# Kernel optimization log

Measured on AMD Instinct MI355X. Metric: run time of the kernel, lower is better.

The kernel has to match this reference:

```python
import jax, jax.numpy as jnp
import numpy as np
import math

N_HEADS = 12
D_MODEL = 768
D_HEAD = 64
IGNORE = -100000.0
INIT_STD = 0.02


def setup_inputs() -> dict:
    key = jax.random.key(0)
    ks = jax.random.split(key, 8)
    b, s = 4, 1024
    return {
        "normalized_resid_pre": jax.random.normal(ks[0], (b, 1, s, D_MODEL), jnp.float32),
        "alt_normalized_resid_pre": jax.random.normal(ks[1], (b, s, D_MODEL), jnp.float32),
        "W_Q": jax.random.normal(ks[2], (N_HEADS, D_MODEL, D_HEAD), jnp.float32) * INIT_STD,
        "b_Q": jnp.zeros((N_HEADS, D_HEAD), jnp.float32),
        "W_K": jax.random.normal(ks[3], (N_HEADS, D_MODEL, D_HEAD), jnp.float32) * INIT_STD,
        "b_K": jnp.zeros((N_HEADS, D_HEAD), jnp.float32),
        "W_V": jax.random.normal(ks[4], (N_HEADS, D_MODEL, D_HEAD), jnp.float32) * INIT_STD,
        "b_V": jnp.zeros((N_HEADS, D_HEAD), jnp.float32),
        "W_O": jax.random.normal(ks[5], (N_HEADS, D_HEAD, D_MODEL), jnp.float32) * INIT_STD,
        "b_O": jnp.zeros((D_MODEL,), jnp.float32),
    }


def _apply_attention(x, W_Q, b_Q, W_K, b_K, W_V, b_V, W_O):
    # x: [batch, n_prev(=2), seq, d_model]
    q = jnp.einsum('bpsd,ndh->bpsnh', x, W_Q) + b_Q
    k = jnp.einsum('bpsd,ndh->bpsnh', x, W_K) + b_K
    v = jnp.einsum('bpsd,ndh->bpsnh', x, W_V) + b_V
    scores = jnp.einsum('bpqnh,bpknh->bpnqk', q, k) / math.sqrt(D_HEAD)
    s = scores.shape[-1]
    causal = jnp.triu(jnp.ones((s, s), bool), k=1)  # True above diagonal
    scores = jnp.where(causal, IGNORE, scores)
    pattern = jax.nn.softmax(scores, axis=-1)
    z = jnp.einsum('bpnqk,bpknh->bpqnh', pattern, v)
    # per-head output, NOT summed over heads: [b, p, q, n, d_model]
    return jnp.einsum('bpqnh,nhd->bpqnd', z, W_O)


def reference(normalized_resid_pre, alt_normalized_resid_pre,
              W_Q, b_Q, W_K, b_K, W_V, b_V, W_O, b_O):
    x = jnp.concatenate(
        [normalized_resid_pre, alt_normalized_resid_pre[:, None]], axis=1)  # [b,2,s,d]
    attn_out = _apply_attention(x, W_Q, b_Q, W_K, b_K, W_V, b_V, W_O)  # [b,2,s,n,d]
    old_ablated = attn_out.sum(axis=-2)  # [b,2,s,d]
    orig = attn_out[:, 1]  # [b,s,n,d]
    alt = attn_out[:, 0]   # [b,s,n,d]
    ablate = jnp.ones((N_HEADS, N_HEADS), attn_out.dtype) - jnp.eye(N_HEADS, dtype=attn_out.dtype)
    new_ablated = jnp.einsum('bqnd,kn->bkqd', orig, ablate) + jnp.transpose(alt, (0, 2, 1, 3))
    return jnp.concatenate([old_ablated, new_ablated], axis=1) + b_O  # [b, 2+n_heads, s, d]
```

## Files before the change

### kernel.cpp

```cpp
#include <hip/hip_runtime.h>
#include <math.h>

#define NH 12
#define DM 768
#define DH 64
#define SS 1024

typedef __attribute__((ext_vector_type(8))) short short8;
typedef __attribute__((ext_vector_type(4))) float floatx4;
typedef __attribute__((ext_vector_type(4))) unsigned short usv4;

__device__ __forceinline__ ushort f2bf(float f) {
    union { float f; unsigned u; } v; v.f = f;
    unsigned r = v.u + 0x7fffu + ((v.u >> 16) & 1u);
    return (ushort)(r >> 16);
}
__device__ __forceinline__ float bf2f(ushort u) {
    union { unsigned u; float f; } v; v.u = ((unsigned)u) << 16;
    return v.f;
}

__device__ __forceinline__ void gld_lds16(const ushort* g, ushort* l) {
    __builtin_amdgcn_global_load_lds(
        (const __attribute__((address_space(1))) unsigned int*)g,
        (__attribute__((address_space(3))) unsigned int*)l, 16, 0, 0);
}


__global__ __launch_bounds__(256) void prep_k(
    const float* __restrict__ x0, const float* __restrict__ x1,
    const float* __restrict__ WQ, const float* __restrict__ WK, const float* __restrict__ WV,
    const float* __restrict__ WO,
    ushort* __restrict__ xb, ushort* __restrict__ WbT, ushort* __restrict__ WObT)
{
    __shared__ float T[64][68];
    const int bid = blockIdx.x;
    const int tid = threadIdx.x;
    if (bid < 3072) {
        const size_t e = ((size_t)bid * 256 + tid) * 8;
        const int m = (int)(e / DM), col = (int)(e % DM);
        const int p = (m >> 10) & 1, b = m >> 11, s = m & 1023;
        const float* src = ((p == 0) ? x0 : x1) + (size_t)b * (SS * DM) + (size_t)s * DM + col;
        float4 v0 = *(const float4*)(src);
        float4 v1 = *(const float4*)(src + 4);
        short8 o;
        o[0] = (short)f2bf(v0.x); o[1] = (short)f2bf(v0.y); o[2] = (short)f2bf(v0.z); o[3] = (short)f2bf(v0.w);
        o[4] = (short)f2bf(v1.x); o[5] = (short)f2bf(v1.y); o[6] = (short)f2bf(v1.z); o[7] = (short)f2bf(v1.w);
        *(short8*)(xb + e) = o;
        return;
    }
    const int di = tid >> 2, cg = tid & 3;
    if (bid < 3072 + 432) {
        const int idx = bid - 3072;
        const int tn = idx % 36, dt = idx / 36;
        const int t = tn / NH, n = tn % NH;
        const float* W = ((t == 0) ? WQ : (t == 1) ? WK : WV) + (size_t)n * (DM * DH);
        const int d0 = dt * 64;
#pragma unroll
        for (int j = 0; j < 4; j++) {
            const int c = cg * 16 + j * 4;
            float4 v = *(const float4*)(W + (size_t)(d0 + di) * DH + c);
            *(float4*)&T[di][c] = v;
        }
        __syncthreads();
        ushort* dst = WbT + (size_t)t * (NH * DH * DM) + (size_t)n * (DH * DM) + (size_t)di * DM + d0;
#pragma unroll
        for (int j = 0; j < 4; j++) {
            const int dc = cg * 16 + j * 4;
            usv4 o;
            o[0] = f2bf(T[dc + 0][di]); o[1] = f2bf(T[dc + 1][di]);
            o[2] = f2bf(T[dc + 2][di]); o[3] = f2bf(T[dc + 3][di]);
            *(usv4*)(dst + dc) = o;
        }
        return;
    }
    {
        const int idx = bid - 3072 - 432;
        const int kt = idx % 12, dt = idx / 12;
#pragma unroll
        for (int j = 0; j < 4; j++) {
            const int c = cg * 16 + j * 4;
            float4 v = *(const float4*)(WO + (size_t)(kt * 64 + di) * DM + dt * 64 + c);
            *(float4*)&T[di][c] = v;
        }
        __syncthreads();
        ushort* dst = WObT + (size_t)(dt * 64 + di) * DM + kt * 64;
#pragma unroll
        for (int j = 0; j < 4; j++) {
            const int dc = cg * 16 + j * 4;
            usv4 o;
            o[0] = f2bf(T[dc + 0][di]); o[1] = f2bf(T[dc + 1][di]);
            o[2] = f2bf(T[dc + 2][di]); o[3] = f2bf(T[dc + 3][di]);
            *(usv4*)(dst + dc) = o;
        }
    }
}

__global__ __launch_bounds__(256) void qkv_mfma_k(
    const ushort* __restrict__ xb, const ushort* __restrict__ WbT,
    const float* __restrict__ bQ, const float* __restrict__ bK, const float* __restrict__ bV,
    ushort* __restrict__ Qb, ushort* __restrict__ Kb, ushort* __restrict__ Vtb)
{
    __shared__ ushort As[128 * 32];
    __shared__ ushort Bs[128 * 32];
    const int tid = threadIdx.x;
    const int w = tid >> 6, lane = tid & 63;
    const int l16 = lane & 15, quad = lane >> 4;
    const int jt = blockIdx.x;
    const int mt = blockIdx.y;
    const int t = jt / 6;
    const int jb = (jt % 6) * 128;
    const int mbase = mt * 128;

    const ushort* Bt = WbT + (size_t)t * (DM * DM) + (size_t)jb * DM;

    const int srow = (lane >> 2);
    const int scol = (lane & 3) * 8;
    const ushort* gA0 = xb + (size_t)(mbase + w * 32 + srow) * DM + scol;
    const ushort* gB0 = Bt + (size_t)(w * 32 + srow) * DM + scol;
    ushort* lA0 = As + (w * 32) * 32;
    ushort* lB0 = Bs + (w * 32) * 32;

    floatx4 acc[2][8];
#pragma unroll
    for (int m = 0; m < 2; m++)
#pragma unroll
        for (int n = 0; n < 8; n++) acc[m][n] = (floatx4){0.f, 0.f, 0.f, 0.f};

    for (int kt = 0; kt < 24; kt++) {
        const int k0 = kt * 32;
        __syncthreads();
        gld_lds16(gA0 + k0, lA0);
        gld_lds16(gA0 + (size_t)16 * DM + k0, lA0 + 16 * 32);
        gld_lds16(gB0 + k0, lB0);
        gld_lds16(gB0 + (size_t)16 * DM + k0, lB0 + 16 * 32);
        asm volatile("s_waitcnt vmcnt(0)" ::: "memory");
        __syncthreads();

        const ushort* Ab = As + (w * 32 + l16) * 32 + quad * 8;
        short8 a0 = *(const short8*)(Ab);
        short8 a1 = *(const short8*)(Ab + 16 * 32);
#pragma unroll
        for (int n = 0; n < 8; n++) {
            short8 b = *(const short8*)(Bs + (n * 16 + l16) * 32 + quad * 8);
            acc[0][n] = __builtin_amdgcn_mfma_f32_16x16x32_bf16(a0, b, acc[0][n], 0, 0, 0);
            acc[1][n] = __builtin_amdgcn_mfma_f32_16x16x32_bf16(a1, b, acc[1][n], 0, 0, 0);
        }
    }

    const float* bias = (t == 0) ? bQ : (t == 1) ? bK : bV;
#pragma unroll
    for (int m = 0; m < 2; m++) {
        const int mrow0 = mbase + w * 32 + m * 16 + quad * 4;
        const int bp = mrow0 >> 10;
        const int s0 = mrow0 & 1023;
#pragma unroll
        for (int n = 0; n < 8; n++) {
            const int col = jb + n * 16 + l16;
            const int head = col >> 6, h = col & 63;
            const size_t hb = ((size_t)bp * NH + head) * (SS * DH);
            const float bv = bias[head * DH + h];
            if (t == 0) {
#pragma unroll
                for (int r = 0; r < 4; r++)
                    Qb[hb + (size_t)(s0 + r) * DH + h] = f2bf((acc[m][n][r] + bv) * 0.125f);
            } else if (t == 1) {
#pragma unroll
                for (int r = 0; r < 4; r++)
                    Kb[hb + (size_t)(s0 + r) * DH + h] = f2bf(acc[m][n][r] + bv);
            } else {
                usv4 o;
#pragma unroll
                for (int r = 0; r < 4; r++) o[r] = f2bf(acc[m][n][r] + bv);
                *(usv4*)(Vtb + hb + (size_t)h * SS + s0) = o;
            }
        }
    }
}

__global__ __launch_bounds__(256) void attn_mfma_k(
    const ushort* __restrict__ Qb, const ushort* __restrict__ Kb,
    const ushort* __restrict__ Vtb, ushort* __restrict__ Zb)
{
    __shared__ __align__(16) ushort Ks[64 * 64];
    __shared__ __align__(16) ushort Vs[64 * 64];
    __shared__ __align__(16) ushort P_lds[4][16][72];

    const int bid  = blockIdx.x;
    const int head = (bid & 7) + ((bid >> 6) << 3);
    const int qpair = (bid >> 3) & 7;
    const int wave = threadIdx.x >> 6;
    const int lane = threadIdx.x & 63;
    const int quad = lane >> 4;
    const int l16  = lane & 15;

    const size_t hb = (size_t)head * (SS * DH);
    const ushort* Qh = Qb + hb;
    const ushort* Kh = Kb + hb;
    const ushort* Vh = Vtb + hb;

    const int srl = lane >> 3;
    const int su  = lane & 7;

#pragma unroll 1
    for (int half = 0; half < 2; half++) {
        const int qtile = (half == 0) ? (15 - qpair) : qpair;
        const int qbase = qtile * 64 + wave * 16;
        const int q_lane = qbase + l16;

        short8 b_q0 = *(const short8*)(Qh + (size_t)(qbase + l16) * DH + quad * 8);
        short8 b_q1 = *(const short8*)(Qh + (size_t)(qbase + l16) * DH + 32 + quad * 8);

        floatx4 o[4];
        float m_run = -1e30f, l_run = 0.f;
#pragma unroll
        for (int hg = 0; hg < 4; hg++) o[hg] = (floatx4){0.f, 0.f, 0.f, 0.f};

        const int kb_last = qtile;
        for (int kb = 0; kb <= kb_last; kb++) {
            __syncthreads();
#pragma unroll
            for (int j = 0; j < 2; j++) {
                const int rl  = j * 8 + srl;
                const int row = wave * 16 + rl;
                const int uu  = su ^ (rl & 7);
                gld_lds16(Kh + (size_t)(kb * 64 + row) * DH + uu * 8,
                          Ks + wave * 1024 + j * 512);
                gld_lds16(Vh + (size_t)row * SS + kb * 64 + uu * 8,
                          Vs + wave * 1024 + j * 512);
            }
            asm volatile("s_waitcnt vmcnt(0)" ::: "memory");
            __syncthreads();

            floatx4 c[4];
#pragma unroll
            for (int kg = 0; kg < 4; kg++) {
                const int r = kg * 16 + l16;
                short8 k0 = *(const short8*)(Ks + r * 64 + ((quad ^ (r & 7)) * 8));
                short8 k1 = *(const short8*)(Ks + r * 64 + (((quad + 4) ^ (r & 7)) * 8));
                floatx4 cc = (floatx4){0.f, 0.f, 0.f, 0.f};
                cc = __builtin_amdgcn_mfma_f32_16x16x32_bf16(k0, b_q0, cc, 0, 0, 0);
                cc = __builtin_amdgcn_mfma_f32_16x16x32_bf16(k1, b_q1, cc, 0, 0, 0);
                c[kg] = cc;
            }
            if (kb == kb_last) {
#pragma unroll
                for (int kg = 0; kg < 4; kg++)
#pragma unroll
                    for (int r = 0; r < 4; r++) {
                        const int key = kb * 64 + kg * 16 + quad * 4 + r;
                        if (key > q_lane) c[kg][r] = -1e30f;
                    }
            }

            float mk0 = fmaxf(fmaxf(c[0][0], c[0][1]), fmaxf(c[0][2], c[0][3]));
            float mk1 = fmaxf(fmaxf(c[1][0], c[1][1]), fmaxf(c[1][2], c[1][3]));
            float mk2 = fmaxf(fmaxf(c[2][0], c[2][1]), fmaxf(c[2][2], c[2][3]));
            float mk3 = fmaxf(fmaxf(c[3][0], c[3][1]), fmaxf(c[3][2], c[3][3]));
            float mt = fmaxf(fmaxf(mk0, mk1), fmaxf(mk2, mk3));
            mt = fmaxf(mt, __shfl_xor(mt, 16, 64));
            mt = fmaxf(mt, __shfl_xor(mt, 32, 64));
            const float m_new = fmaxf(m_run, mt);
            const float alpha = __expf(m_run - m_new);
            m_run = m_new;

            float rs = 0.f;
#pragma unroll
            for (int kg = 0; kg < 4; kg++) {
                const float p0 = __expf(c[kg][0] - m_new);
                const float p1 = __expf(c[kg][1] - m_new);
                const float p2 = __expf(c[kg][2] - m_new);
                const float p3 = __expf(c[kg][3] - m_new);
                rs += (p0 + p1) + (p2 + p3);
                const unsigned w0 = ((unsigned)f2bf(p1) << 16) | (unsigned)f2bf(p0);
                const unsigned w1 = ((unsigned)f2bf(p3) << 16) | (unsigned)f2bf(p2);
                *(unsigned*)&P_lds[wave][l16][kg * 16 + quad * 4]     = w0;
                *(unsigned*)&P_lds[wave][l16][kg * 16 + quad * 4 + 2] = w1;
            }
            rs += __shfl_xor(rs, 16, 64);
            rs += __shfl_xor(rs, 32, 64);
            l_run = l_run * alpha + rs;

            float a_o[4];
#pragma unroll
            for (int r = 0; r < 4; r++) a_o[r] = __shfl(alpha, quad * 4 + r, 64);
#pragma unroll
            for (int hg = 0; hg < 4; hg++)
#pragma unroll
                for (int r = 0; r < 4; r++) o[hg][r] *= a_o[r];

            asm volatile("s_waitcnt lgkmcnt(0)" ::: "memory");
            short8 ap0 = *(const short8*)&P_lds[wave][l16][quad * 8];
            short8 ap1 = *(const short8*)&P_lds[wave][l16][32 + quad * 8];
#pragma unroll
            for (int hg = 0; hg < 4; hg++) {
                const int h = hg * 16 + l16;
                short8 bv0 = *(const short8*)(Vs + h * 64 + ((quad ^ (h & 7)) * 8));
                short8 bv1 = *(const short8*)(Vs + h * 64 + (((quad + 4) ^ (h & 7)) * 8));
                o[hg] = __builtin_amdgcn_mfma_f32_16x16x32_bf16(ap0, bv0, o[hg], 0, 0, 0);
                o[hg] = __builtin_amdgcn_mfma_f32_16x16x32_bf16(ap1, bv1, o[hg], 0, 0, 0);
            }
            asm volatile("s_waitcnt lgkmcnt(0)" ::: "memory");
        }

        const float inv = 1.f / l_run;
        float inv_o[4];
#pragma unroll
        for (int r = 0; r < 4; r++) inv_o[r] = __shfl(inv, quad * 4 + r, 64);
#pragma unroll
        for (int hg = 0; hg < 4; hg++)
#pragma unroll
            for (int r = 0; r < 4; r++)
                Zb[hb + (size_t)(qbase + quad * 4 + r) * DH + hg * 16 + l16] = f2bf(o[hg][r] * inv_o[r]);
    }
}

__global__ __launch_bounds__(256) void zdiff_k(
    const ushort* __restrict__ Zb, ushort* __restrict__ Zd)
{
    const size_t e = ((size_t)blockIdx.x * 256 + threadIdx.x) * 8;
    const int bk = (int)(e >> 16);
    const int off = (int)(e & 65535);
    const int b_ = bk / NH, k = bk % NH;
    const ushort* z0 = Zb + ((size_t)(b_ * 2) * NH + k) * (SS * DH) + off;
    const ushort* z1 = Zb + ((size_t)(b_ * 2 + 1) * NH + k) * (SS * DH) + off;
    short8 a = *(const short8*)z0;
    short8 c = *(const short8*)z1;
    short8 o;
#pragma unroll
    for (int i = 0; i < 8; i++)
        o[i] = (short)f2bf(bf2f((ushort)a[i]) - bf2f((ushort)c[i]));
    *(short8*)(Zd + e) = o;
}

__global__ __launch_bounds__(256) void outproj_k(
    const ushort* __restrict__ Zb, const ushort* __restrict__ Zd,
    const ushort* __restrict__ WObT, const float* __restrict__ bO,
    float* __restrict__ out)
{
    __shared__ ushort As[64 * 32];
    __shared__ ushort Bs[128 * 32];
    const int tid = threadIdx.x;
    const int w = tid >> 6, lane = tid & 63;
    const int l16 = lane & 15, quad = lane >> 4;
    const int jb = blockIdx.x * 128;
    const int q0 = blockIdx.y * 64;
    const int b_ = blockIdx.z;

    const int srow = lane >> 2;
    const int scol = (lane & 3) * 8;
    const int arow = q0 + w * 16 + srow;
    const ushort* gB = WObT + (size_t)(jb + w * 32 + srow) * DM + scol;
    ushort* lA = As + (w * 16) * 32;
    ushort* lB0 = Bs + (w * 32) * 32;
    ushort* lB1 = Bs + (w * 32 + 16) * 32;

    const ushort* Afrag = As + (w * 16 + l16) * 32 + quad * 8;

    float bia[8];
#pragma unroll
    for (int n = 0; n < 8; n++) bia[n] = bO[jb + n * 16 + l16];

    floatx4 s1[8];
#pragma unroll 1
    for (int pp = 0; pp < 2; pp++) {
        const ushort* Zp = Zb + (size_t)(b_ * 2 + pp) * (NH * SS * DH);
        floatx4 acc[8];
#pragma unroll
        for (int n = 0; n < 8; n++) acc[n] = (floatx4){0.f, 0.f, 0.f, 0.f};
        for (int kt = 0; kt < 24; kt++) {
            const int k0 = kt * 32;
            __syncthreads();
            gld_lds16(Zp + (size_t)(k0 >> 6) * (SS * DH) + (size_t)arow * DH + (k0 & 63) + scol, lA);
            gld_lds16(gB + k0, lB0);
            gld_lds16(gB + (size_t)16 * DM + k0, lB1);
            asm volatile("s_waitcnt vmcnt(0)" ::: "memory");
            __syncthreads();
            short8 a = *(const short8*)(Afrag);
#pragma unroll
            for (int n = 0; n < 8; n++) {
                short8 b = *(const short8*)(Bs + (n * 16 + l16) * 32 + quad * 8);
                acc[n] = __builtin_amdgcn_mfma_f32_16x16x32_bf16(a, b, acc[n], 0, 0, 0);
            }
        }
        float* obase = out + ((size_t)(b_ * 14 + pp) * SS) * DM;
        const int qr = q0 + w * 16 + quad * 4;
#pragma unroll
        for (int n = 0; n < 8; n++) {
            const int d = jb + n * 16 + l16;
#pragma unroll
            for (int r = 0; r < 4; r++) {
                const float v = acc[n][r] + bia[n];
                obase[(size_t)(qr + r) * DM + d] = v;
                if (pp == 1) s1[n][r] = v;
            }
        }
    }

    const ushort* Zdb = Zd + (size_t)b_ * (NH * SS * DH);
#pragma unroll 1
    for (int k = 0; k < NH; k++) {
        const ushort* Zdk = Zdb + (size_t)k * (SS * DH);
        floatx4 acc[8];
#pragma unroll
        for (int n = 0; n < 8; n++) acc[n] = (floatx4){0.f, 0.f, 0.f, 0.f};
#pragma unroll
        for (int kt = 0; kt < 2; kt++) {
            const int k0 = kt * 32;
            __syncthreads();
            gld_lds16(Zdk + (size_t)arow * DH + k0 + scol, lA);
            gld_lds16(gB + k * DH + k0, lB0);
            gld_lds16(gB + (size_t)16 * DM + k * DH + k0, lB1);
            asm volatile("s_waitcnt vmcnt(0)" ::: "memory");
            __syncthreads();
            short8 a = *(const short8*)(Afrag);
#pragma unroll
            for (int n = 0; n < 8; n++) {
                short8 b = *(const short8*)(Bs + (n * 16 + l16) * 32 + quad * 8);
                acc[n] = __builtin_amdgcn_mfma_f32_16x16x32_bf16(a, b, acc[n], 0, 0, 0);
            }
        }
        float* obase = out + ((size_t)(b_ * 14 + 2 + k) * SS) * DM;
        const int qr = q0 + w * 16 + quad * 4;
#pragma unroll
        for (int n = 0; n < 8; n++) {
            const int d = jb + n * 16 + l16;
#pragma unroll
            for (int r = 0; r < 4; r++)
                obase[(size_t)(qr + r) * DM + d] = acc[n][r] + s1[n][r];
        }
    }
}

extern "C" void kernel_launch(void* const* d_in, const int* in_sizes, int n_in,
                              void* d_out, int out_size, void* d_ws, size_t ws_size,
                              hipStream_t stream)
{
    const float* x0 = (const float*)d_in[0];
    const float* x1 = (const float*)d_in[1];
    const float* WQ = (const float*)d_in[2];
    const float* bQ = (const float*)d_in[3];
    const float* WK = (const float*)d_in[4];
    const float* bK = (const float*)d_in[5];
    const float* WV = (const float*)d_in[6];
    const float* bV = (const float*)d_in[7];
    const float* WO = (const float*)d_in[8];
    const float* bO = (const float*)d_in[9];
    float* out = (float*)d_out;

    ushort* ub   = (ushort*)d_ws;
    ushort* Qb   = ub;
    ushort* Kb   = Qb + 6291456;
    ushort* Vtb  = Kb + 6291456;
    ushort* xb   = Vtb + 6291456;
    ushort* WbT  = xb + 6291456;
    ushort* Zb   = WbT + 1769472;
    ushort* WObT = Zb + 6291456;
    ushort* Zd   = WObT + 589824;

    prep_k<<<dim3(3648), 256, 0, stream>>>(x0, x1, WQ, WK, WV, WO, xb, WbT, WObT);
    qkv_mfma_k<<<dim3(18, 64), 256, 0, stream>>>(xb, WbT, bQ, bK, bV, Qb, Kb, Vtb);
    attn_mfma_k<<<dim3(768), 256, 0, stream>>>(Qb, Kb, Vtb, Zb);
    zdiff_k<<<dim3(1536), 256, 0, stream>>>(Zb, Zd);
    outproj_k<<<dim3(6, 16, 4), 256, 0, stream>>>(Zb, Zd, WObT, bO, out);
}
```

Baseline: 354.1 us.

## Double-buffer LDS tiles in QKV and output-projection GEMM kernels

Adds two LDS buffers to the QKV projection and output projection kernels. The next K-slice is loaded asynchronously into one buffer while MFMAs run on the other, so global-to-LDS latency is hidden behind compute and one barrier per iteration is removed. The per-head ablation loop in outproj is flattened into a single 24-step pipelined loop with stores at every second step. The cost is twice the LDS footprint, which may lower occupancy.

```diff
diff --git a/kernel.cpp b/kernel.cpp
--- a/kernel.cpp
+++ b/kernel.cpp
@@ -101,8 +101,8 @@
     const float* __restrict__ bQ, const float* __restrict__ bK, const float* __restrict__ bV,
     ushort* __restrict__ Qb, ushort* __restrict__ Kb, ushort* __restrict__ Vtb)
 {
-    __shared__ ushort As[128 * 32];
-    __shared__ ushort Bs[128 * 32];
+    __shared__ ushort As[2 * 128 * 32];
+    __shared__ ushort Bs[2 * 128 * 32];
     const int tid = threadIdx.x;
     const int w = tid >> 6, lane = tid & 63;
     const int l16 = lane & 15, quad = lane >> 4;
@@ -127,25 +127,37 @@
 #pragma unroll
         for (int n = 0; n < 8; n++) acc[m][n] = (floatx4){0.f, 0.f, 0.f, 0.f};
 
+    gld_lds16(gA0, lA0);
+    gld_lds16(gA0 + (size_t)16 * DM, lA0 + 16 * 32);
+    gld_lds16(gB0, lB0);
+    gld_lds16(gB0 + (size_t)16 * DM, lB0 + 16 * 32);
+    asm volatile("s_waitcnt vmcnt(0)" ::: "memory");
+    __syncthreads();
+
+    int cur = 0;
+#pragma unroll 2
     for (int kt = 0; kt < 24; kt++) {
-        const int k0 = kt * 32;
-        __syncthreads();
-        gld_lds16(gA0 + k0, lA0);
-        gld_lds16(gA0 + (size_t)16 * DM + k0, lA0 + 16 * 32);
-        gld_lds16(gB0 + k0, lB0);
-        gld_lds16(gB0 + (size_t)16 * DM + k0, lB0 + 16 * 32);
+        if (kt < 23) {
+            const int k1 = (kt + 1) * 32;
+            const int nb = (cur ^ 1) * 4096;
+            gld_lds16(gA0 + k1, lA0 + nb);
+            gld_lds16(gA0 + (size_t)16 * DM + k1, lA0 + nb + 16 * 32);
+            gld_lds16(gB0 + k1, lB0 + nb);
+            gld_lds16(gB0 + (size_t)16 * DM + k1, lB0 + nb + 16 * 32);
+        }
+        const int cb = cur * 4096;
+        const ushort* Ab = As + cb + (w * 32 + l16) * 32 + quad * 8;
+        short8 a0 = *(const short8*)(Ab);
+        short8 a1 = *(const short8*)(Ab + 16 * 32);
+#pragma unroll
+        for (int n = 0; n < 8; n++) {
+            short8 b = *(const short8*)(Bs + cb + (n * 16 + l16) * 32 + quad * 8);
+            acc[0][n] = __builtin_amdgcn_mfma_f32_16x16x32_bf16(a0, b, acc[0][n], 0, 0, 0);
+            acc[1][n] = __builtin_amdgcn_mfma_f32_16x16x32_bf16(a1, b, acc[1][n], 0, 0, 0);
+        }
         asm volatile("s_waitcnt vmcnt(0)" ::: "memory");
         __syncthreads();
-
-        const ushort* Ab = As + (w * 32 + l16) * 32 + quad * 8;
-        short8 a0 = *(const short8*)(Ab);
-        short8 a1 = *(const short8*)(Ab + 16 * 32);
-#pragma unroll
-        for (int n = 0; n < 8; n++) {
-            short8 b = *(const short8*)(Bs + (n * 16 + l16) * 32 + quad * 8);
-            acc[0][n] = __builtin_amdgcn_mfma_f32_16x16x32_bf16(a0, b, acc[0][n], 0, 0, 0);
-            acc[1][n] = __builtin_amdgcn_mfma_f32_16x16x32_bf16(a1, b, acc[1][n], 0, 0, 0);
-        }
+        cur ^= 1;
     }
 
     const float* bias = (t == 0) ? bQ : (t == 1) ? bK : bV;
@@ -338,8 +350,8 @@
     const ushort* __restrict__ WObT, const float* __restrict__ bO,
     float* __restrict__ out)
 {
-    __shared__ ushort As[64 * 32];
-    __shared__ ushort Bs[128 * 32];
+    __shared__ ushort As[2 * 64 * 32];
+    __shared__ ushort Bs[2 * 128 * 32];
     const int tid = threadIdx.x;
     const int w = tid >> 6, lane = tid & 63;
     const int l16 = lane & 15, quad = lane >> 4;
@@ -351,15 +363,16 @@
     const int scol = (lane & 3) * 8;
     const int arow = q0 + w * 16 + srow;
     const ushort* gB = WObT + (size_t)(jb + w * 32 + srow) * DM + scol;
-    ushort* lA = As + (w * 16) * 32;
+    ushort* lA  = As + (w * 16) * 32;
     ushort* lB0 = Bs + (w * 32) * 32;
     ushort* lB1 = Bs + (w * 32 + 16) * 32;
 
-    const ushort* Afrag = As + (w * 16 + l16) * 32 + quad * 8;
-
     float bia[8];
 #pragma unroll
     for (int n = 0; n < 8; n++) bia[n] = bO[jb + n * 16 + l16];
+
+    const int qr = q0 + w * 16 + quad * 4;
+    int cur = 0;
 
     floatx4 s1[8];
 #pragma unroll 1
@@ -368,23 +381,34 @@
         floatx4 acc[8];
 #pragma unroll
         for (int n = 0; n < 8; n++) acc[n] = (floatx4){0.f, 0.f, 0.f, 0.f};
+
+        gld_lds16(Zp + (size_t)arow * DH + scol, lA + cur * 2048);
+        gld_lds16(gB, lB0 + cur * 4096);
+        gld_lds16(gB + (size_t)16 * DM, lB1 + cur * 4096);
+        asm volatile("s_waitcnt vmcnt(0)" ::: "memory");
+        __syncthreads();
+
+#pragma unroll 2
         for (int kt = 0; kt < 24; kt++) {
-            const int k0 = kt * 32;
-            __syncthreads();
-            gld_lds16(Zp + (size_t)(k0 >> 6) * (SS * DH) + (size_t)arow * DH + (k0 & 63) + scol, lA);
-            gld_lds16(gB + k0, lB0);
-            gld_lds16(gB + (size_t)16 * DM + k0, lB1);
+            if (kt < 23) {
+                const int k1 = kt + 1;
+                const int na = (cur ^ 1) * 2048, nb = (cur ^ 1) * 4096;
+                gld_lds16(Zp + (size_t)(k1 >> 1) * (SS * DH) + (size_t)arow * DH + (k1 & 1) * 32 + scol, lA + na);
+                gld_lds16(gB + k1 * 32, lB0 + nb);
+                gld_lds16(gB + (size_t)16 * DM + k1 * 32, lB1 + nb);
+            }
+            const int ca = cur * 2048, cb = cur * 4096;
+            short8 a = *(const short8*)(As + ca + (w * 16 + l16) * 32 + quad * 8);
+#pragma unroll
+            for (int n = 0; n < 8; n++) {
+                short8 b = *(const short8*)(Bs + cb + (n * 16 + l16) * 32 + quad * 8);
+                acc[n] = __builtin_amdgcn_mfma_f32_16x16x32_bf16(a, b, acc[n], 0, 0, 0);
+            }
             asm volatile("s_waitcnt vmcnt(0)" ::: "memory");
             __syncthreads();
-            short8 a = *(const short8*)(Afrag);
-#pragma unroll
-            for (int n = 0; n < 8; n++) {
-                short8 b = *(const short8*)(Bs + (n * 16 + l16) * 32 + quad * 8);
-                acc[n] = __builtin_amdgcn_mfma_f32_16x16x32_bf16(a, b, acc[n], 0, 0, 0);
-            }
+            cur ^= 1;
         }
         float* obase = out + ((size_t)(b_ * 14 + pp) * SS) * DM;
-        const int qr = q0 + w * 16 + quad * 4;
 #pragma unroll
         for (int n = 0; n < 8; n++) {
             const int d = jb + n * 16 + l16;
@@ -398,36 +422,49 @@
     }
 
     const ushort* Zdb = Zd + (size_t)b_ * (NH * SS * DH);
-#pragma unroll 1
-    for (int k = 0; k < NH; k++) {
-        const ushort* Zdk = Zdb + (size_t)k * (SS * DH);
+    {
+        gld_lds16(Zdb + (size_t)arow * DH + scol, lA + cur * 2048);
+        gld_lds16(gB, lB0 + cur * 4096);
+        gld_lds16(gB + (size_t)16 * DM, lB1 + cur * 4096);
+        asm volatile("s_waitcnt vmcnt(0)" ::: "memory");
+        __syncthreads();
+
         floatx4 acc[8];
-#pragma unroll
-        for (int n = 0; n < 8; n++) acc[n] = (floatx4){0.f, 0.f, 0.f, 0.f};
-#pragma unroll
-        for (int kt = 0; kt < 2; kt++) {
-            const int k0 = kt * 32;
-            __syncthreads();
-            gld_lds16(Zdk + (size_t)arow * DH + k0 + scol, lA);
-            gld_lds16(gB + k * DH + k0, lB0);
-            gld_lds16(gB + (size_t)16 * DM + k * DH + k0, lB1);
+#pragma unroll 2
+        for (int i = 0; i < 24; i++) {
+            const int k = i >> 1, kt = i & 1;
+            if (i < 23) {
+                const int k2 = (i + 1) >> 1, kt2 = (i + 1) & 1;
+                const int off = k2 * DH + kt2 * 32;
+                const int na = (cur ^ 1) * 2048, nb = (cur ^ 1) * 4096;
+                gld_lds16(Zdb + (size_t)k2 * (SS * DH) + (size_t)arow * DH + kt2 * 32 + scol, lA + na);
+                gld_lds16(gB + off, lB0 + nb);
+                gld_lds16(gB + (size_t)16 * DM + off, lB1 + nb);
+            }
+            if (kt == 0) {
+#pragma unroll
+                for (int n = 0; n < 8; n++) acc[n] = (floatx4){0.f, 0.f, 0.f, 0.f};
+            }
+            const int ca = cur * 2048, cb = cur * 4096;
+            short8 a = *(const short8*)(As + ca + (w * 16 + l16) * 32 + quad * 8);
+#pragma unroll
+            for (int n = 0; n < 8; n++) {
+                short8 b = *(const short8*)(Bs + cb + (n * 16 + l16) * 32 + quad * 8);
+                acc[n] = __builtin_amdgcn_mfma_f32_16x16x32_bf16(a, b, acc[n], 0, 0, 0);
+            }
+            if (kt == 1) {
+                float* obase = out + ((size_t)(b_ * 14 + 2 + k) * SS) * DM;
+#pragma unroll
+                for (int n = 0; n < 8; n++) {
+                    const int d = jb + n * 16 + l16;
+#pragma unroll
+                    for (int r = 0; r < 4; r++)
+                        obase[(size_t)(qr + r) * DM + d] = acc[n][r] + s1[n][r];
+                }
+            }
             asm volatile("s_waitcnt vmcnt(0)" ::: "memory");
             __syncthreads();
-            short8 a = *(const short8*)(Afrag);
-#pragma unroll
-            for (int n = 0; n < 8; n++) {
-                short8 b = *(const short8*)(Bs + (n * 16 + l16) * 32 + quad * 8);
-                acc[n] = __builtin_amdgcn_mfma_f32_16x16x32_bf16(a, b, acc[n], 0, 0, 0);
-            }
-        }
-        float* obase = out + ((size_t)(b_ * 14 + 2 + k) * SS) * DM;
-        const int qr = q0 + w * 16 + quad * 4;
-#pragma unroll
-        for (int n = 0; n < 8; n++) {
-            const int d = jb + n * 16 + l16;
-#pragma unroll
-            for (int r = 0; r < 4; r++)
-                obase[(size_t)(qr + r) * DM + d] = acc[n][r] + s1[n][r];
+            cur ^= 1;
         }
     }
 }
```

Result: no change. 359.7 us (+1.6%).

## Split output projection into two wider-grid kernels and use 64-wide K tiles

Applied to the files above, without the earlier changes.

The fused output-projection kernel, which ran only 384 blocks and looped serially over the two prefixes and twelve heads, is split into two kernels. One computes the two old_ablated slices with 768 blocks. The other computes each head's ablated output with 4608 blocks, reading the prefix-1 result back from the output buffer instead of keeping it in registers. The QKV GEMM and both projection kernels now stage 64-wide K tiles, which halves the number of barrier-separated load rounds per tile. The cost is more shared memory per block, an extra global read of the s1 slice for every head, and one additional kernel launch.

```diff
diff --git a/kernel.cpp b/kernel.cpp
--- a/kernel.cpp
+++ b/kernel.cpp
@@ -101,8 +101,8 @@
     const float* __restrict__ bQ, const float* __restrict__ bK, const float* __restrict__ bV,
     ushort* __restrict__ Qb, ushort* __restrict__ Kb, ushort* __restrict__ Vtb)
 {
-    __shared__ ushort As[128 * 32];
-    __shared__ ushort Bs[128 * 32];
+    __shared__ ushort As[128 * 64];
+    __shared__ ushort Bs[128 * 64];
     const int tid = threadIdx.x;
     const int w = tid >> 6, lane = tid & 63;
     const int l16 = lane & 15, quad = lane >> 4;
@@ -114,12 +114,8 @@
 
     const ushort* Bt = WbT + (size_t)t * (DM * DM) + (size_t)jb * DM;
 
-    const int srow = (lane >> 2);
-    const int scol = (lane & 3) * 8;
-    const ushort* gA0 = xb + (size_t)(mbase + w * 32 + srow) * DM + scol;
-    const ushort* gB0 = Bt + (size_t)(w * 32 + srow) * DM + scol;
-    ushort* lA0 = As + (w * 32) * 32;
-    ushort* lB0 = Bs + (w * 32) * 32;
+    const int sr8 = lane >> 3;
+    const int su8 = lane & 7;
 
     floatx4 acc[2][8];
 #pragma unroll
@@ -127,24 +123,29 @@
 #pragma unroll
         for (int n = 0; n < 8; n++) acc[m][n] = (floatx4){0.f, 0.f, 0.f, 0.f};
 
-    for (int kt = 0; kt < 24; kt++) {
-        const int k0 = kt * 32;
-        __syncthreads();
-        gld_lds16(gA0 + k0, lA0);
-        gld_lds16(gA0 + (size_t)16 * DM + k0, lA0 + 16 * 32);
-        gld_lds16(gB0 + k0, lB0);
-        gld_lds16(gB0 + (size_t)16 * DM + k0, lB0 + 16 * 32);
+    for (int kt = 0; kt < 12; kt++) {
+        const int k0 = kt * 64;
+        __syncthreads();
+#pragma unroll
+        for (int j = 0; j < 4; j++) {
+            const int row = w * 32 + j * 8 + sr8;
+            gld_lds16(xb + (size_t)(mbase + row) * DM + k0 + su8 * 8, As + (w * 32 + j * 8) * 64);
+            gld_lds16(Bt + (size_t)row * DM + k0 + su8 * 8,           Bs + (w * 32 + j * 8) * 64);
+        }
         asm volatile("s_waitcnt vmcnt(0)" ::: "memory");
         __syncthreads();
 
-        const ushort* Ab = As + (w * 32 + l16) * 32 + quad * 8;
-        short8 a0 = *(const short8*)(Ab);
-        short8 a1 = *(const short8*)(Ab + 16 * 32);
-#pragma unroll
-        for (int n = 0; n < 8; n++) {
-            short8 b = *(const short8*)(Bs + (n * 16 + l16) * 32 + quad * 8);
-            acc[0][n] = __builtin_amdgcn_mfma_f32_16x16x32_bf16(a0, b, acc[0][n], 0, 0, 0);
-            acc[1][n] = __builtin_amdgcn_mfma_f32_16x16x32_bf16(a1, b, acc[1][n], 0, 0, 0);
+#pragma unroll
+        for (int kk = 0; kk < 2; kk++) {
+            const ushort* Ab = As + (w * 32 + l16) * 64 + kk * 32 + quad * 8;
+            short8 a0 = *(const short8*)(Ab);
+            short8 a1 = *(const short8*)(Ab + 16 * 64);
+#pragma unroll
+            for (int n = 0; n < 8; n++) {
+                short8 b = *(const short8*)(Bs + (n * 16 + l16) * 64 + kk * 32 + quad * 8);
+                acc[0][n] = __builtin_amdgcn_mfma_f32_16x16x32_bf16(a0, b, acc[0][n], 0, 0, 0);
+                acc[1][n] = __builtin_amdgcn_mfma_f32_16x16x32_bf16(a1, b, acc[1][n], 0, 0, 0);
+            }
         }
     }
 
@@ -333,101 +334,124 @@
     *(short8*)(Zd + e) = o;
 }
 
-__global__ __launch_bounds__(256) void outproj_k(
-    const ushort* __restrict__ Zb, const ushort* __restrict__ Zd,
-    const ushort* __restrict__ WObT, const float* __restrict__ bO,
-    float* __restrict__ out)
-{
-    __shared__ ushort As[64 * 32];
-    __shared__ ushort Bs[128 * 32];
+__global__ __launch_bounds__(256) void outproj1_k(
+    const ushort* __restrict__ Zb, const ushort* __restrict__ WObT,
+    const float* __restrict__ bO, float* __restrict__ out)
+{
+    __shared__ ushort As[64 * 64];
+    __shared__ ushort Bs[128 * 64];
     const int tid = threadIdx.x;
     const int w = tid >> 6, lane = tid & 63;
     const int l16 = lane & 15, quad = lane >> 4;
     const int jb = blockIdx.x * 128;
     const int q0 = blockIdx.y * 64;
-    const int b_ = blockIdx.z;
-
-    const int srow = lane >> 2;
-    const int scol = (lane & 3) * 8;
-    const int arow = q0 + w * 16 + srow;
-    const ushort* gB = WObT + (size_t)(jb + w * 32 + srow) * DM + scol;
-    ushort* lA = As + (w * 16) * 32;
-    ushort* lB0 = Bs + (w * 32) * 32;
-    ushort* lB1 = Bs + (w * 32 + 16) * 32;
-
-    const ushort* Afrag = As + (w * 16 + l16) * 32 + quad * 8;
-
-    float bia[8];
-#pragma unroll
-    for (int n = 0; n < 8; n++) bia[n] = bO[jb + n * 16 + l16];
-
-    floatx4 s1[8];
-#pragma unroll 1
-    for (int pp = 0; pp < 2; pp++) {
-        const ushort* Zp = Zb + (size_t)(b_ * 2 + pp) * (NH * SS * DH);
-        floatx4 acc[8];
-#pragma unroll
-        for (int n = 0; n < 8; n++) acc[n] = (floatx4){0.f, 0.f, 0.f, 0.f};
-        for (int kt = 0; kt < 24; kt++) {
-            const int k0 = kt * 32;
-            __syncthreads();
-            gld_lds16(Zp + (size_t)(k0 >> 6) * (SS * DH) + (size_t)arow * DH + (k0 & 63) + scol, lA);
-            gld_lds16(gB + k0, lB0);
-            gld_lds16(gB + (size_t)16 * DM + k0, lB1);
-            asm volatile("s_waitcnt vmcnt(0)" ::: "memory");
-            __syncthreads();
-            short8 a = *(const short8*)(Afrag);
+    const int b_ = blockIdx.z >> 1;
+    const int pp = blockIdx.z & 1;
+
+    const ushort* Zp = Zb + (size_t)(b_ * 2 + pp) * (NH * SS * DH);
+    const int sr8 = lane >> 3;
+    const int su8 = lane & 7;
+
+    floatx4 acc[8];
+#pragma unroll
+    for (int n = 0; n < 8; n++) acc[n] = (floatx4){0.f, 0.f, 0.f, 0.f};
+
+    for (int kt = 0; kt < 12; kt++) {
+        const int k0 = kt * 64;
+        __syncthreads();
+#pragma unroll
+        for (int j = 0; j < 2; j++) {
+            const int row = w * 16 + j * 8 + sr8;
+            gld_lds16(Zp + (size_t)kt * (SS * DH) + (size_t)(q0 + row) * DH + su8 * 8,
+                      As + (w * 16 + j * 8) * 64);
+        }
+#pragma unroll
+        for (int j = 0; j < 4; j++) {
+            const int row = w * 32 + j * 8 + sr8;
+            gld_lds16(WObT + (size_t)(jb + row) * DM + k0 + su8 * 8,
+                      Bs + (w * 32 + j * 8) * 64);
+        }
+        asm volatile("s_waitcnt vmcnt(0)" ::: "memory");
+        __syncthreads();
+
+#pragma unroll
+        for (int kk = 0; kk < 2; kk++) {
+            short8 a = *(const short8*)(As + (w * 16 + l16) * 64 + kk * 32 + quad * 8);
 #pragma unroll
             for (int n = 0; n < 8; n++) {
-                short8 b = *(const short8*)(Bs + (n * 16 + l16) * 32 + quad * 8);
+                short8 b = *(const short8*)(Bs + (n * 16 + l16) * 64 + kk * 32 + quad * 8);
                 acc[n] = __builtin_amdgcn_mfma_f32_16x16x32_bf16(a, b, acc[n], 0, 0, 0);
             }
         }
-        float* obase = out + ((size_t)(b_ * 14 + pp) * SS) * DM;
-        const int qr = q0 + w * 16 + quad * 4;
+    }
+
+    float* obase = out + ((size_t)(b_ * 14 + pp) * SS) * DM;
+    const int qr = q0 + w * 16 + quad * 4;
+#pragma unroll
+    for (int n = 0; n < 8; n++) {
+        const int d = jb + n * 16 + l16;
+        const float bv = bO[d];
+#pragma unroll
+        for (int r = 0; r < 4; r++)
+            obase[(size_t)(qr + r) * DM + d] = acc[n][r] + bv;
+    }
+}
+
+__global__ __launch_bounds__(256) void outproj2_k(
+    const ushort* __restrict__ Zd, const ushort* __restrict__ WObT,
+    const float* __restrict__ out_s1, float* __restrict__ out)
+{
+    __shared__ ushort As[64 * 64];
+    __shared__ ushort Bs[128 * 64];
+    const int tid = threadIdx.x;
+    const int w = tid >> 6, lane = tid & 63;
+    const int l16 = lane & 15, quad = lane >> 4;
+    const int jb = blockIdx.x * 128;
+    const int q0 = blockIdx.y * 64;
+    const int b_ = blockIdx.z / NH;
+    const int k  = blockIdx.z % NH;
+
+    const ushort* Zdk = Zd + (size_t)(b_ * NH + k) * (SS * DH);
+    const int sr8 = lane >> 3;
+    const int su8 = lane & 7;
+
+#pragma unroll
+    for (int j = 0; j < 2; j++) {
+        const int row = w * 16 + j * 8 + sr8;
+        gld_lds16(Zdk + (size_t)(q0 + row) * DH + su8 * 8, As + (w * 16 + j * 8) * 64);
+    }
+#pragma unroll
+    for (int j = 0; j < 4; j++) {
+        const int row = w * 32 + j * 8 + sr8;
+        gld_lds16(WObT + (size_t)(jb + row) * DM + k * DH + su8 * 8,
+                  Bs + (w * 32 + j * 8) * 64);
+    }
+    asm volatile("s_waitcnt vmcnt(0)" ::: "memory");
+    __syncthreads();
+
+    floatx4 acc[8];
+#pragma unroll
+    for (int n = 0; n < 8; n++) acc[n] = (floatx4){0.f, 0.f, 0.f, 0.f};
+#pragma unroll
+    for (int kk = 0; kk < 2; kk++) {
+        short8 a = *(const short8*)(As + (w * 16 + l16) * 64 + kk * 32 + quad * 8);
 #pragma unroll
         for (int n = 0; n < 8; n++) {
-            const int d = jb + n * 16 + l16;
-#pragma unroll
-            for (int r = 0; r < 4; r++) {
-                const float v = acc[n][r] + bia[n];
-                obase[(size_t)(qr + r) * DM + d] = v;
-                if (pp == 1) s1[n][r] = v;
-            }
-        }
-    }
-
-    const ushort* Zdb = Zd + (size_t)b_ * (NH * SS * DH);
-#pragma unroll 1
-    for (int k = 0; k < NH; k++) {
-        const ushort* Zdk = Zdb + (size_t)k * (SS * DH);
-        floatx4 acc[8];
-#pragma unroll
-        for (int n = 0; n < 8; n++) acc[n] = (floatx4){0.f, 0.f, 0.f, 0.f};
-#pragma unroll
-        for (int kt = 0; kt < 2; kt++) {
-            const int k0 = kt * 32;
-            __syncthreads();
-            gld_lds16(Zdk + (size_t)arow * DH + k0 + scol, lA);
-            gld_lds16(gB + k * DH + k0, lB0);
-            gld_lds16(gB + (size_t)16 * DM + k * DH + k0, lB1);
-            asm volatile("s_waitcnt vmcnt(0)" ::: "memory");
-            __syncthreads();
-            short8 a = *(const short8*)(Afrag);
-#pragma unroll
-            for (int n = 0; n < 8; n++) {
-                short8 b = *(const short8*)(Bs + (n * 16 + l16) * 32 + quad * 8);
-                acc[n] = __builtin_amdgcn_mfma_f32_16x16x32_bf16(a, b, acc[n], 0, 0, 0);
-            }
-        }
-        float* obase = out + ((size_t)(b_ * 14 + 2 + k) * SS) * DM;
-        const int qr = q0 + w * 16 + quad * 4;
-#pragma unroll
-        for (int n = 0; n < 8; n++) {
-            const int d = jb + n * 16 + l16;
-#pragma unroll
-            for (int r = 0; r < 4; r++)
-                obase[(size_t)(qr + r) * DM + d] = acc[n][r] + s1[n][r];
+            short8 b = *(const short8*)(Bs + (n * 16 + l16) * 64 + kk * 32 + quad * 8);
+            acc[n] = __builtin_amdgcn_mfma_f32_16x16x32_bf16(a, b, acc[n], 0, 0, 0);
+        }
+    }
+
+    const int qr = q0 + w * 16 + quad * 4;
+    const float* s1base = out_s1 + ((size_t)(b_ * 14 + 1) * SS) * DM;
+    float* obase = out + ((size_t)(b_ * 14 + 2 + k) * SS) * DM;
+#pragma unroll
+    for (int n = 0; n < 8; n++) {
+        const int d = jb + n * 16 + l16;
+#pragma unroll
+        for (int r = 0; r < 4; r++) {
+            const float s1 = s1base[(size_t)(qr + r) * DM + d];
+            obase[(size_t)(qr + r) * DM + d] = acc[n][r] + s1;
         }
     }
 }
@@ -462,5 +486,6 @@
     qkv_mfma_k<<<dim3(18, 64), 256, 0, stream>>>(xb, WbT, bQ, bK, bV, Qb, Kb, Vtb);
     attn_mfma_k<<<dim3(768), 256, 0, stream>>>(Qb, Kb, Vtb, Zb);
     zdiff_k<<<dim3(1536), 256, 0, stream>>>(Zb, Zd);
-    outproj_k<<<dim3(6, 16, 4), 256, 0, stream>>>(Zb, Zd, WObT, bO, out);
-}
+    outproj1_k<<<dim3(6, 16, 8), 256, 0, stream>>>(Zb, WObT, bO, out);
+    outproj2_k<<<dim3(6, 16, 48), 256, 0, stream>>>(Zd, WObT, out, out);
+}
```

New measurement: 380.1 us. 7.3% more time.
